# Kernel tuning notes

Measured on AMD Instinct MI355X. Metric: run time of the kernel, lower is better.

## Reference

```python
import jax, jax.numpy as jnp
import numpy as np

B, T, D, H, K = 128, 128, 2048, 512, 512
KSIZES = (2, 3, 4, 5)
OUT_DIM = 2048
IN_DIM = 2 * H + len(KSIZES) * K + D  # 5120
BN_EPS = 1e-5


def _gru_dir(x, w_ih, w_hh, b_ih, b_hh):
    """Single-direction torch-style GRU. x: [B,T,D] -> [B,T,H]."""
    xw = jnp.einsum('btd,gd->btg', x, w_ih) + b_ih  # precompute input proj [B,T,3H]
    h0 = jnp.zeros((x.shape[0], w_hh.shape[1]), x.dtype)

    def step(h, xw_t):
        gh = h @ w_hh.T + b_hh
        xr, xz, xn = jnp.split(xw_t, 3, axis=-1)
        hr, hz, hn = jnp.split(gh, 3, axis=-1)
        r = jax.nn.sigmoid(xr + hr)
        z = jax.nn.sigmoid(xz + hz)
        n = jnp.tanh(xn + r * hn)
        h_new = (1.0 - z) * n + z * h
        return h_new, h_new

    _, hs = jax.lax.scan(step, h0, jnp.swapaxes(xw, 0, 1))
    return jnp.swapaxes(hs, 0, 1)


def _forward(videos, videos_origin, videos_mask, lengths,
             w_ih_f, w_hh_f, b_ih_f, b_hh_f,
             w_ih_b, w_hh_b, b_ih_b, b_hh_b,
             conv_w2, conv_b2, conv_w3, conv_b3, conv_w4, conv_b4, conv_w5, conv_b5,
             fc_w, fc_b, bn_gamma, bn_beta, bn_mean, bn_var):
    # bidirectional GRU on the full padded sequence (torch code does NOT pack)
    fwd = _gru_dir(videos, w_ih_f, w_hh_f, b_ih_f, b_hh_f)
    bwd = _gru_dir(videos[:, ::-1], w_ih_b, w_hh_b, b_ih_b, b_hh_b)[:, ::-1]
    gru_init = jnp.concatenate([fwd, bwd], axis=-1)  # [B,T,2H]

    # fused masked mean (replaces per-sample python loop): mean over first lengths[i] steps
    masked = gru_init * videos_mask[:, :, None]
    mean_gru = masked.sum(axis=1) / lengths.astype(gru_init.dtype)[:, None]  # [B,2H]

    # multi-scale text-CNN over masked GRU outputs
    x4 = masked[:, None, :, :]  # [B,1,T,2H]
    cons = []
    for w, cw, cb in zip(KSIZES, (conv_w2, conv_w3, conv_w4, conv_w5),
                         (conv_b2, conv_b3, conv_b4, conv_b5)):
        y = jax.lax.conv_general_dilated(
            x4, cw, window_strides=(1, 1), padding=[(w - 1, w - 1), (0, 0)],
            dimension_numbers=('NCHW', 'OIHW', 'NCHW'))  # [B,K,T+w-1,1]
        y = jax.nn.relu(y + cb[None, :, None, None])
        cons.append(y.max(axis=(2, 3)))  # global max-pool over time
    con_out = jnp.concatenate(cons, axis=1)  # [B, 4K]

    # concate == 'full' ; dropout is identity at inference
    feats = jnp.concatenate([mean_gru, con_out, videos_origin], axis=1)  # [B,5120]
    feats = feats @ fc_w + fc_b
    feats = bn_gamma * (feats - bn_mean) / jnp.sqrt(bn_var + BN_EPS) + bn_beta
    # l2norm over feature dim
    feats = feats / jnp.sqrt(jnp.sum(feats * feats, axis=1, keepdims=True))
    return feats


def setup_inputs() -> dict:
    key = jax.random.key(0)
    ks = jax.random.split(key, 32)
    s = 0.02
    inp = {
        'videos': jax.random.normal(ks[0], (B, T, D), jnp.float32),
        'videos_origin': jax.random.normal(ks[1], (B, D), jnp.float32),
    }
    lengths = jax.random.randint(ks[2], (B,), 1, T + 1).astype(jnp.int64)
    inp['lengths'] = lengths
    inp['videos_mask'] = (jnp.arange(T)[None, :] < lengths[:, None]).astype(jnp.float32)
    inp['w_ih_f'] = jax.random.normal(ks[3], (3 * H, D), jnp.float32) * s
    inp['w_hh_f'] = jax.random.normal(ks[4], (3 * H, H), jnp.float32) * s
    inp['b_ih_f'] = jnp.zeros((3 * H,), jnp.float32)
    inp['b_hh_f'] = jnp.zeros((3 * H,), jnp.float32)
    inp['w_ih_b'] = jax.random.normal(ks[5], (3 * H, D), jnp.float32) * s
    inp['w_hh_b'] = jax.random.normal(ks[6], (3 * H, H), jnp.float32) * s
    inp['b_ih_b'] = jnp.zeros((3 * H,), jnp.float32)
    inp['b_hh_b'] = jnp.zeros((3 * H,), jnp.float32)
    for i, w in enumerate(KSIZES):
        inp[f'conv_w{w}'] = jax.random.normal(ks[7 + i], (K, 1, w, 2 * H), jnp.float32) * s
        inp[f'conv_b{w}'] = jnp.zeros((K,), jnp.float32)
    inp['fc_w'] = jax.random.normal(ks[12], (IN_DIM, OUT_DIM), jnp.float32) * s
    inp['fc_b'] = jnp.zeros((OUT_DIM,), jnp.float32)
    inp['bn_gamma'] = jnp.ones((OUT_DIM,), jnp.float32)
    inp['bn_beta'] = jnp.zeros((OUT_DIM,), jnp.float32)
    inp['bn_mean'] = jnp.zeros((OUT_DIM,), jnp.float32)
    inp['bn_var'] = jnp.ones((OUT_DIM,), jnp.float32)
    return inp


def reference(videos, videos_origin, lengths, videos_mask,
              w_ih_f, w_hh_f, b_ih_f, b_hh_f,
              w_ih_b, w_hh_b, b_ih_b, b_hh_b,
              conv_w2, conv_b2, conv_w3, conv_b3, conv_w4, conv_b4, conv_w5, conv_b5,
              fc_w, fc_b, bn_gamma, bn_beta, bn_mean, bn_var):
    return _forward(videos, videos_origin, videos_mask, lengths,
                    w_ih_f, w_hh_f, b_ih_f, b_hh_f,
                    w_ih_b, w_hh_b, b_ih_b, b_hh_b,
                    conv_w2, conv_b2, conv_w3, conv_b3, conv_w4, conv_b4, conv_w5, conv_b5,
                    fc_w, fc_b, bn_gamma, bn_beta, bn_mean, bn_var)
```

## Files before the change

### kernel.cpp

```cpp
#include <hip/hip_runtime.h>
#include <stdint.h>

#define B_   128
#define T_   128
#define D_   2048
#define H_   512
#define G3   1536
#define CH   1024
#define KC   512
#define OUTD 2048
#define IND  5120
#define TP   168
#define MPAD 160

typedef short vb8 __attribute__((ext_vector_type(8)));
typedef float v4f __attribute__((ext_vector_type(4)));

__device__ __forceinline__ unsigned short f2b(float f) {
  unsigned u = __float_as_uint(f);
  u = (u + 0x7FFFu + ((u >> 16) & 1u)) >> 16;
  return (unsigned short)u;
}
__device__ __forceinline__ float b2f(unsigned short u) {
  return __uint_as_float((unsigned)u << 16);
}

__device__ __forceinline__ void gl16(const unsigned short* g, unsigned short* l) {
  __builtin_amdgcn_global_load_lds(
      (const __attribute__((address_space(1))) void*)g,
      (__attribute__((address_space(3))) void*)l, 16, 0, 0);
}

__global__ void k_cvt(const float* __restrict__ in, unsigned short* __restrict__ out, int n4) {
  int stride = gridDim.x * blockDim.x;
  for (int i = blockIdx.x * blockDim.x + threadIdx.x; i < n4; i += stride) {
    float4 v = reinterpret_cast<const float4*>(in)[i];
    ushort4 o;
    o.x = f2b(v.x); o.y = f2b(v.y); o.z = f2b(v.z); o.w = f2b(v.w);
    reinterpret_cast<ushort4*>(out)[i] = o;
  }
}

__global__ void k_tcvt(const float* __restrict__ in, unsigned short* __restrict__ out) {
  __shared__ float tile[32][33];
  const int tx = threadIdx.x & 31;
  const int ty = threadIdx.x >> 5;
  const int n0 = blockIdx.x * 32;
  const int k0 = blockIdx.y * 32;
#pragma unroll
  for (int i = 0; i < 4; ++i)
    tile[ty + 8 * i][tx] = in[(size_t)(k0 + ty + 8 * i) * OUTD + n0 + tx];
  __syncthreads();
#pragma unroll
  for (int i = 0; i < 4; ++i)
    out[(size_t)(n0 + ty + 8 * i) * IND + k0 + tx] = f2b(tile[tx][ty + 8 * i]);
}

template<int EPI, int CB>
__global__ __launch_bounds__(256) void k_gemm(
    const unsigned short* __restrict__ A,
    const unsigned short* __restrict__ Bm,
    const float* __restrict__ bias,
    void* __restrict__ Cv,
    int K, int lda, int ldc, int convw)
{
  __shared__ unsigned short sA[128 * 32];
  __shared__ unsigned short sB[128 * 32];
  float*          C32 = (float*)Cv;
  unsigned short* C16 = (unsigned short*)Cv;

  const int m0 = blockIdx.x * 128;
  const int n0 = blockIdx.y * 128;

  const int tid  = threadIdx.x;
  const int lane = tid & 63;
  const int wv   = tid >> 6;
  const int wr   = wv >> 1;
  const int wc   = wv & 1;

  const unsigned short* ag[2];
  const unsigned short* bg[2];
  unsigned short* al[2];
  unsigned short* bl[2];
#pragma unroll
  for (int q = 0; q < 2; ++q) {
    int c  = wv * 2 + q;
    int r  = c * 16 + (lane >> 2);
    int kc = (lane & 3) * 8;
    long abase;
    if (EPI == 1) {
      int m   = m0 + r;
      int b   = m / MPAD;
      int tau = m - b * MPAD;
      abase = (long)(b * TP + 4 + tau - (convw - 1)) * CH;
    } else {
      abase = (long)(m0 + r) * lda;
    }
    ag[q] = A + abase + kc;
    bg[q] = Bm + (long)(n0 + r) * K + kc;
    al[q] = sA + c * 512;
    bl[q] = sB + c * 512;
  }

  v4f acc[4][4] = {};
  const int kq = (lane >> 4) * 8;
  const int fr = lane & 15;

  for (int k0 = 0; k0 < K; k0 += 32) {
    if (k0) __syncthreads();
#pragma unroll
    for (int q = 0; q < 2; ++q) {
      gl16(ag[q] + k0, al[q]);
      gl16(bg[q] + k0, bl[q]);
    }
    __syncthreads();
    vb8 af[4], bfr[4];
#pragma unroll
    for (int i = 0; i < 4; ++i) {
      af[i]  = *reinterpret_cast<const vb8*>(sA + (wr * 64 + i * 16 + fr) * 32 + kq);
      bfr[i] = *reinterpret_cast<const vb8*>(sB + (wc * 64 + i * 16 + fr) * 32 + kq);
    }
#pragma unroll
    for (int i = 0; i < 4; ++i)
#pragma unroll
      for (int j = 0; j < 4; ++j)
        acc[i][j] = __builtin_amdgcn_mfma_f32_16x16x32_bf16(af[i], bfr[j], acc[i][j], 0, 0, 0);
  }

  const int rl = lane >> 4;
#pragma unroll
  for (int i = 0; i < 4; ++i) {
#pragma unroll
    for (int j = 0; j < 4; ++j) {
      int col = n0 + wc * 64 + j * 16 + fr;
      float bs = bias[col];
      if (EPI == 0) {
#pragma unroll
        for (int r = 0; r < 4; ++r) {
          int m = m0 + wr * 64 + i * 16 + rl * 4 + r;
          float v = acc[i][j][r] + bs;
          if (CB) C16[(long)m * ldc + col] = f2b(v);
          else    C32[(long)m * ldc + col] = v;
        }
      } else if (EPI == 2) {
        const int dirb = col >= G3;
        const int xcol = col - dirb * G3;
        unsigned short* base = C16 + (size_t)dirb * ((size_t)B_ * T_ * G3);
#pragma unroll
        for (int r = 0; r < 4; ++r) {
          int m = m0 + wr * 64 + i * 16 + rl * 4 + r;
          base[(long)m * G3 + xcol] = f2b(acc[i][j][r] + bs);
        }
      } else {
        int mf = m0 + wr * 64 + i * 16;
        int b  = mf / MPAD;
        int tf = mf - b * MPAD;
        float mx = 0.f;
#pragma unroll
        for (int r = 0; r < 4; ++r) {
          int tau = tf + rl * 4 + r;
          float v = acc[i][j][r] + bs;
          v = v > 0.f ? v : 0.f;
          if (tau < T_ + convw - 1) mx = v > mx ? v : mx;
        }
        mx = fmaxf(mx, __shfl_xor(mx, 16));
        mx = fmaxf(mx, __shfl_xor(mx, 32));
        if (rl == 0 && tf < T_ + convw - 1)
          atomicMax(reinterpret_cast<int*>(C32 + (long)b * ldc + col), __float_as_int(mx));
      }
    }
  }
}

__global__ __launch_bounds__(512) void k_scan(
    const unsigned short* __restrict__ whh16,
    const float* __restrict__ bhhf, const float* __restrict__ bhhb,
    const unsigned short* __restrict__ xw,
    const int* __restrict__ lengths,
    unsigned short* __restrict__ hbuf,
    unsigned short* __restrict__ xpad,
    float* __restrict__ meang,
    unsigned int* __restrict__ cnt)
{
  __shared__ unsigned short sw[96 * 512];
  const int wg   = blockIdx.x;
  const int dir  = wg >> 4;
  const int u0   = (wg & 15) * 32;
  const int tid  = threadIdx.x;
  const int lane = tid & 63;
  const int wv   = tid >> 6;
  const int fr   = lane & 15;
  const int rl   = lane >> 4;
  const int kq   = rl * 8;

  const unsigned short* Wd  = whh16 + (size_t)dir * (3 * H_ * H_);
  const float*          bhh = dir ? bhhb : bhhf;
  const unsigned short* xwd = xw + (size_t)dir * ((size_t)B_ * T_ * G3);
  unsigned short* hb = hbuf + dir * (2 * B_ * H_);
  unsigned int* mycnt = cnt + dir * 64;

  for (int i = tid; i < 96 * 64; i += 512) {
    int row  = i >> 6;
    int slot = i & 63;
    const unsigned short* src = Wd + (size_t)((row >> 5) * H_ + u0 + (row & 31)) * H_ + slot * 8;
    *reinterpret_cast<vb8*>((char*)sw + ((row * 1024 + slot * 16) ^ ((row & 7) << 4))) =
        *reinterpret_cast<const vb8*>(src);
  }
  __syncthreads();

  int mylen[4];
#pragma unroll
  for (int r = 0; r < 4; ++r) mylen[r] = lengths[wv * 16 + rl * 4 + r];

  float bh[3][2];
#pragma unroll
  for (int g = 0; g < 3; ++g)
#pragma unroll
    for (int j = 0; j < 2; ++j) bh[g][j] = bhh[g * H_ + u0 + j * 16 + fr];

  float hst[8], macc[8];
#pragma unroll
  for (int i = 0; i < 8; ++i) { hst[i] = 0.f; macc[i] = 0.f; }

  unsigned short uxw[3][2][4];
  {
    const int t0 = dir ? (T_ - 1) : 0;
#pragma unroll
    for (int g = 0; g < 3; ++g)
#pragma unroll
      for (int j = 0; j < 2; ++j)
#pragma unroll
        for (int r = 0; r < 4; ++r)
          uxw[g][j][r] = xwd[((size_t)(wv * 16 + rl * 4 + r) * T_ + t0) * G3 +
                             g * H_ + u0 + j * 16 + fr];
  }

  for (int s = 0; s < T_; ++s) {
    const int t = dir ? (T_ - 1 - s) : s;

    v4f acc[3][2] = {};
    if (s > 0) {
      const unsigned short* arow = hb + ((s - 1) & 1) * (B_ * H_) + (wv * 16 + fr) * H_;
#pragma unroll 4
      for (int ks = 0; ks < 16; ++ks) {
        vb8 a = *reinterpret_cast<const vb8*>(arow + ks * 32 + kq);
#pragma unroll
        for (int g = 0; g < 3; ++g)
#pragma unroll
          for (int j = 0; j < 2; ++j) {
            vb8 wf = *reinterpret_cast<const vb8*>(
                (const char*)sw +
                (((g * 32 + j * 16 + fr) * 1024 + ks * 64 + rl * 16) ^ ((fr & 7) << 4)));
            acc[g][j] = __builtin_amdgcn_mfma_f32_16x16x32_bf16(a, wf, acc[g][j], 0, 0, 0);
          }
      }
    }

    unsigned short* hc = hb + (s & 1) * (B_ * H_);
#pragma unroll
    for (int j = 0; j < 2; ++j)
#pragma unroll
      for (int r = 0; r < 4; ++r) {
        const int idx = j * 4 + r;
        const int b   = wv * 16 + rl * 4 + r;
        const int u   = u0 + j * 16 + fr;
        float xr = b2f(uxw[0][j][r]), xz = b2f(uxw[1][j][r]), xn = b2f(uxw[2][j][r]);
        float hr = acc[0][j][r] + bh[0][j];
        float hz = acc[1][j][r] + bh[1][j];
        float hn = acc[2][j][r] + bh[2][j];
        float rr = 1.f / (1.f + __expf(-(xr + hr)));
        float z  = 1.f / (1.f + __expf(-(xz + hz)));
        float ax = xn + rr * hn;
        float n  = 2.f / (1.f + __expf(-2.f * ax)) - 1.f;
        float h  = (1.f - z) * n + z * hst[idx];
        hst[idx] = h;
        hc[b * H_ + u] = f2b(h);
        if (t < mylen[r]) {
          xpad[((size_t)b * TP + 4 + t) * CH + dir * H_ + u] = f2b(h);
          macc[idx] += h;
        }
      }

    if (s < T_ - 1) {
      const int tn = dir ? (T_ - 2 - s) : (s + 1);
#pragma unroll
      for (int g = 0; g < 3; ++g)
#pragma unroll
        for (int j = 0; j < 2; ++j)
#pragma unroll
          for (int r = 0; r < 4; ++r)
            uxw[g][j][r] = xwd[((size_t)(wv * 16 + rl * 4 + r) * T_ + tn) * G3 +
                               g * H_ + u0 + j * 16 + fr];
      __syncthreads();
      if (tid == 0) {
        __hip_atomic_fetch_add(mycnt, 1u, __ATOMIC_RELEASE, __HIP_MEMORY_SCOPE_AGENT);
        const unsigned tgt = (unsigned)(s + 1) * 16;
        while (__hip_atomic_load(mycnt, __ATOMIC_RELAXED, __HIP_MEMORY_SCOPE_AGENT) < tgt)
          __builtin_amdgcn_s_sleep(1);
        __builtin_amdgcn_fence(__ATOMIC_ACQUIRE, "agent");
      }
      __syncthreads();
    }
  }

#pragma unroll
  for (int j = 0; j < 2; ++j)
#pragma unroll
    for (int r = 0; r < 4; ++r)
      meang[(size_t)(wv * 16 + rl * 4 + r) * CH + dir * H_ + u0 + j * 16 + fr] =
          macc[j * 4 + r] / (float)mylen[r];
}

__global__ void k_feats(const float* __restrict__ mg, const float* __restrict__ co,
                        const float* __restrict__ vo, unsigned short* __restrict__ out) {
  int i = blockIdx.x * 256 + threadIdx.x;
  int b = i / IND, c = i - b * IND;
  float v;
  if (c < CH) v = mg[b * CH + c];
  else if (c < CH + OUTD) v = co[b * OUTD + (c - CH)];
  else v = vo[b * D_ + (c - CH - OUTD)];
  out[i] = f2b(v);
}

__global__ __launch_bounds__(256) void k_bnnorm(const float* __restrict__ x,
    const float* __restrict__ g, const float* __restrict__ bt,
    const float* __restrict__ mn, const float* __restrict__ vr,
    float* __restrict__ out) {
  const int b = blockIdx.x;
  __shared__ float red[4];
  float vals[8];
  float ss = 0.f;
#pragma unroll
  for (int i = 0; i < 8; ++i) {
    int c = threadIdx.x + i * 256;
    float y = g[c] * (x[(size_t)b * OUTD + c] - mn[c]) / sqrtf(vr[c] + 1e-5f) + bt[c];
    vals[i] = y;
    ss += y * y;
  }
#pragma unroll
  for (int s2 = 1; s2 < 64; s2 <<= 1) ss += __shfl_xor(ss, s2);
  if ((threadIdx.x & 63) == 0) red[threadIdx.x >> 6] = ss;
  __syncthreads();
  float inv = 1.f / sqrtf(red[0] + red[1] + red[2] + red[3]);
#pragma unroll
  for (int i = 0; i < 8; ++i)
    out[(size_t)b * OUTD + threadIdx.x + i * 256] = vals[i] * inv;
}

extern "C" void kernel_launch(void* const* d_in, const int* in_sizes, int n_in,
                              void* d_out, int out_size, void* d_ws, size_t ws_size,
                              hipStream_t stream) {
  (void)in_sizes; (void)n_in; (void)out_size; (void)ws_size;
  const float* videos = (const float*)d_in[0];
  const float* vorig  = (const float*)d_in[1];
  const int*   lens   = (const int*)d_in[2];
  const float* wihf = (const float*)d_in[4];
  const float* whhf = (const float*)d_in[5];
  const float* bihf = (const float*)d_in[6];
  const float* bhhf = (const float*)d_in[7];
  const float* wihb = (const float*)d_in[8];
  const float* whhb = (const float*)d_in[9];
  const float* bihb = (const float*)d_in[10];
  const float* bhhb = (const float*)d_in[11];
  const float* cw[4] = {(const float*)d_in[12], (const float*)d_in[14],
                        (const float*)d_in[16], (const float*)d_in[18]};
  const float* cb[4] = {(const float*)d_in[13], (const float*)d_in[15],
                        (const float*)d_in[17], (const float*)d_in[19]};
  const float* fcw = (const float*)d_in[20];
  const float* fcb = (const float*)d_in[21];
  const float* bng = (const float*)d_in[22];
  const float* bnb = (const float*)d_in[23];
  const float* bnm = (const float*)d_in[24];
  const float* bnv = (const float*)d_in[25];
  float* out = (float*)d_out;

  char* ws = (char*)d_ws;
  size_t off = 0;
  auto alloc = [&](size_t bytes) -> void* {
    void* p = ws + off;
    off = (off + bytes + 255) & ~(size_t)255;
    return p;
  };
  unsigned int*   cnt    = (unsigned int*)alloc(1024);
  unsigned short* xw16   = (unsigned short*)alloc((size_t)2 * B_ * T_ * G3 * 2);
  unsigned short* whh16  = (unsigned short*)alloc((size_t)2 * 3 * H_ * H_ * 2);
  unsigned short* hbuf   = (unsigned short*)alloc((size_t)2 * 2 * B_ * H_ * 2);
  float*          meang  = (float*)alloc((size_t)B_ * CH * 4);
  float*          conout = (float*)alloc((size_t)B_ * OUTD * 4);
  unsigned short* feats  = (unsigned short*)alloc((size_t)B_ * IND * 2);
  float*          fcout  = (float*)alloc((size_t)B_ * OUTD * 4);
  unsigned short* wihcat = (unsigned short*)alloc((size_t)2 * G3 * D_ * 2);
  unsigned short* cw16   = (unsigned short*)alloc((size_t)KC * 14 * CH * 2);
  unsigned short* vid16  = (unsigned short*)alloc((size_t)B_ * T_ * D_ * 2);
  float*          biascat= (float*)alloc(2 * G3 * 4);
  unsigned short* xpad = vid16;
  unsigned short* fcT  = vid16 + (size_t)B_ * TP * CH;

  hipMemsetAsync(cnt, 0, 1024, stream);
  hipMemsetAsync(conout, 0, (size_t)B_ * OUTD * 4, stream);
  hipMemcpyAsync(biascat,      bihf, G3 * 4, hipMemcpyDeviceToDevice, stream);
  hipMemcpyAsync(biascat + G3, bihb, G3 * 4, hipMemcpyDeviceToDevice, stream);

  k_cvt<<<2048, 256, 0, stream>>>(videos, vid16, B_ * T_ * D_ / 4);
  k_cvt<<<512, 256, 0, stream>>>(wihf, wihcat, G3 * D_ / 4);
  k_cvt<<<512, 256, 0, stream>>>(wihb, wihcat + (size_t)G3 * D_, G3 * D_ / 4);
  k_cvt<<<768, 256, 0, stream>>>(whhf, whh16, 3 * H_ * H_ / 4);
  k_cvt<<<768, 256, 0, stream>>>(whhb, whh16 + (size_t)3 * H_ * H_, 3 * H_ * H_ / 4);
  {
    size_t cwoff = 0;
    for (int i = 0; i < 4; ++i) {
      int w = i + 2;
      int n = KC * w * CH;
      k_cvt<<<256, 256, 0, stream>>>(cw[i], cw16 + cwoff, n / 4);
      cwoff += (size_t)n;
    }
  }

  k_gemm<2, 1><<<dim3(128, 24), 256, 0, stream>>>(vid16, wihcat, biascat, xw16, D_, D_, 0, 0);

  hipMemsetAsync(xpad, 0, (size_t)B_ * TP * CH * 2, stream);
  k_tcvt<<<dim3(64, 160), 256, 0, stream>>>(fcw, fcT);

  k_scan<<<dim3(32), dim3(512), 0, stream>>>(whh16, bhhf, bhhb, xw16, lens,
                                             hbuf, xpad, meang, cnt);

  {
    size_t cwoff = 0;
    for (int i = 0; i < 4; ++i) {
      int w = i + 2;
      k_gemm<1, 0><<<dim3(160, 4), 256, 0, stream>>>(xpad, cw16 + cwoff, cb[i],
                                                     conout + i * KC, w * CH, 0, OUTD, w);
      cwoff += (size_t)KC * w * CH;
    }
  }

  k_feats<<<2560, 256, 0, stream>>>(meang, conout, vorig, feats);
  k_gemm<0, 0><<<dim3(1, 16), 256, 0, stream>>>(feats, fcT, fcb, fcout, IND, IND, OUTD, 0);
  k_bnnorm<<<B_, 256, 0, stream>>>(fcout, bng, bnb, bnm, bnv, out);
}
```

Before: 1.934 ms.

## Batch conv GEMMs into one launch, trim padding, split-K the FC GEMM

The four text-CNN conv GEMM launches become a single launch, with grid z selecting the kernel width, its weight offset and a concatenated bias. The per-sample row padding drops from 160 to 144, which still covers T+w-1 for every width and cuts wasted tile rows. The FC GEMM, which ran on only 16 workgroups, now splits K four ways into separate fp32 partial buffers. The batchnorm/normalize kernel sums those partials and adds the FC bias, at the cost of extra partial-buffer traffic.

Result: faster. 1.830 ms (-5.4%).

```diff
diff --git a/kernel.cpp b/kernel.cpp
--- a/kernel.cpp
+++ b/kernel.cpp
@@ -11,7 +11,7 @@
 #define OUTD 2048
 #define IND  5120
 #define TP   168
-#define MPAD 160
+#define MPAD 144
 
 typedef short vb8 __attribute__((ext_vector_type(8)));
 typedef float v4f __attribute__((ext_vector_type(4)));
@@ -71,6 +71,23 @@
 
   const int m0 = blockIdx.x * 128;
   const int n0 = blockIdx.y * 128;
+  const int cz = blockIdx.z;
+
+  int K_ = K;
+  int w_ = convw;
+  int koff = 0;
+  const unsigned short* Bm_ = Bm;
+  const float* bias_ = bias;
+  if (EPI == 1) {
+    constexpr int cum[4] = {0, 2, 5, 9};
+    w_   = cz + 2;
+    K_   = w_ * CH;
+    Bm_  = Bm + (size_t)cum[cz] * KC * CH;
+    bias_ = bias + cz * KC;
+  } else if (EPI == 3) {
+    koff = cz * K;
+  }
+  const int bstride = (EPI == 3) ? convw : K_;
 
   const int tid  = threadIdx.x;
   const int lane = tid & 63;
@@ -92,12 +109,12 @@
       int m   = m0 + r;
       int b   = m / MPAD;
       int tau = m - b * MPAD;
-      abase = (long)(b * TP + 4 + tau - (convw - 1)) * CH;
+      abase = (long)(b * TP + 4 + tau - (w_ - 1)) * CH;
     } else {
-      abase = (long)(m0 + r) * lda;
+      abase = (long)(m0 + r) * lda + koff;
     }
     ag[q] = A + abase + kc;
-    bg[q] = Bm + (long)(n0 + r) * K + kc;
+    bg[q] = Bm_ + (long)(n0 + r) * bstride + kc + koff;
     al[q] = sA + c * 512;
     bl[q] = sB + c * 512;
   }
@@ -106,7 +123,7 @@
   const int kq = (lane >> 4) * 8;
   const int fr = lane & 15;
 
-  for (int k0 = 0; k0 < K; k0 += 32) {
+  for (int k0 = 0; k0 < K_; k0 += 32) {
     if (k0) __syncthreads();
 #pragma unroll
     for (int q = 0; q < 2; ++q) {
@@ -133,7 +150,7 @@
 #pragma unroll
     for (int j = 0; j < 4; ++j) {
       int col = n0 + wc * 64 + j * 16 + fr;
-      float bs = bias[col];
+      float bs = (EPI == 3) ? 0.f : bias_[col];
       if (EPI == 0) {
 #pragma unroll
         for (int r = 0; r < 4; ++r) {
@@ -151,6 +168,12 @@
           int m = m0 + wr * 64 + i * 16 + rl * 4 + r;
           base[(long)m * G3 + xcol] = f2b(acc[i][j][r] + bs);
         }
+      } else if (EPI == 3) {
+#pragma unroll
+        for (int r = 0; r < 4; ++r) {
+          int m = m0 + wr * 64 + i * 16 + rl * 4 + r;
+          C32[(size_t)cz * (B_ * OUTD) + (long)m * ldc + col] = acc[i][j][r];
+        }
       } else {
         int mf = m0 + wr * 64 + i * 16;
         int b  = mf / MPAD;
@@ -161,12 +184,13 @@
           int tau = tf + rl * 4 + r;
           float v = acc[i][j][r] + bs;
           v = v > 0.f ? v : 0.f;
-          if (tau < T_ + convw - 1) mx = v > mx ? v : mx;
+          if (tau < T_ + w_ - 1) mx = v > mx ? v : mx;
         }
         mx = fmaxf(mx, __shfl_xor(mx, 16));
         mx = fmaxf(mx, __shfl_xor(mx, 32));
-        if (rl == 0 && tf < T_ + convw - 1)
-          atomicMax(reinterpret_cast<int*>(C32 + (long)b * ldc + col), __float_as_int(mx));
+        if (rl == 0 && tf < T_ + w_ - 1)
+          atomicMax(reinterpret_cast<int*>(C32 + (long)b * ldc + cz * KC + col),
+                    __float_as_int(mx));
       }
     }
   }
@@ -323,17 +347,21 @@
 }
 
 __global__ __launch_bounds__(256) void k_bnnorm(const float* __restrict__ x,
+    const float* __restrict__ fcb,
     const float* __restrict__ g, const float* __restrict__ bt,
     const float* __restrict__ mn, const float* __restrict__ vr,
     float* __restrict__ out) {
   const int b = blockIdx.x;
+  const size_t PL = (size_t)B_ * OUTD;
   __shared__ float red[4];
   float vals[8];
   float ss = 0.f;
 #pragma unroll
   for (int i = 0; i < 8; ++i) {
     int c = threadIdx.x + i * 256;
-    float y = g[c] * (x[(size_t)b * OUTD + c] - mn[c]) / sqrtf(vr[c] + 1e-5f) + bt[c];
+    size_t o = (size_t)b * OUTD + c;
+    float xs = x[o] + x[PL + o] + x[2 * PL + o] + x[3 * PL + o] + fcb[c];
+    float y = g[c] * (xs - mn[c]) / sqrtf(vr[c] + 1e-5f) + bt[c];
     vals[i] = y;
     ss += y * y;
   }
@@ -388,11 +416,12 @@
   float*          meang  = (float*)alloc((size_t)B_ * CH * 4);
   float*          conout = (float*)alloc((size_t)B_ * OUTD * 4);
   unsigned short* feats  = (unsigned short*)alloc((size_t)B_ * IND * 2);
-  float*          fcout  = (float*)alloc((size_t)B_ * OUTD * 4);
+  float*          fcpart = (float*)alloc((size_t)4 * B_ * OUTD * 4);
   unsigned short* wihcat = (unsigned short*)alloc((size_t)2 * G3 * D_ * 2);
   unsigned short* cw16   = (unsigned short*)alloc((size_t)KC * 14 * CH * 2);
   unsigned short* vid16  = (unsigned short*)alloc((size_t)B_ * T_ * D_ * 2);
   float*          biascat= (float*)alloc(2 * G3 * 4);
+  float*          cbcat  = (float*)alloc(4 * KC * 4);
   unsigned short* xpad = vid16;
   unsigned short* fcT  = vid16 + (size_t)B_ * TP * CH;
 
@@ -400,6 +429,8 @@
   hipMemsetAsync(conout, 0, (size_t)B_ * OUTD * 4, stream);
   hipMemcpyAsync(biascat,      bihf, G3 * 4, hipMemcpyDeviceToDevice, stream);
   hipMemcpyAsync(biascat + G3, bihb, G3 * 4, hipMemcpyDeviceToDevice, stream);
+  for (int i = 0; i < 4; ++i)
+    hipMemcpyAsync(cbcat + i * KC, cb[i], KC * 4, hipMemcpyDeviceToDevice, stream);
 
   k_cvt<<<2048, 256, 0, stream>>>(videos, vid16, B_ * T_ * D_ / 4);
   k_cvt<<<512, 256, 0, stream>>>(wihf, wihcat, G3 * D_ / 4);
@@ -424,17 +455,10 @@
   k_scan<<<dim3(32), dim3(512), 0, stream>>>(whh16, bhhf, bhhb, xw16, lens,
                                              hbuf, xpad, meang, cnt);
 
-  {
-    size_t cwoff = 0;
-    for (int i = 0; i < 4; ++i) {
-      int w = i + 2;
-      k_gemm<1, 0><<<dim3(160, 4), 256, 0, stream>>>(xpad, cw16 + cwoff, cb[i],
-                                                     conout + i * KC, w * CH, 0, OUTD, w);
-      cwoff += (size_t)KC * w * CH;
-    }
-  }
+  k_gemm<1, 0><<<dim3(144, 4, 4), 256, 0, stream>>>(xpad, cw16, cbcat, conout, 0, 0, OUTD, 0);
 
   k_feats<<<2560, 256, 0, stream>>>(meang, conout, vorig, feats);
-  k_gemm<0, 0><<<dim3(1, 16), 256, 0, stream>>>(feats, fcT, fcb, fcout, IND, IND, OUTD, 0);
-  k_bnnorm<<<B_, 256, 0, stream>>>(fcout, bng, bnb, bnm, bnv, out);
-}
+  k_gemm<3, 0><<<dim3(1, 16, 4), 256, 0, stream>>>(feats, fcT, fcb, fcpart,
+                                                   IND / 4, IND, OUTD, IND);
+  k_bnnorm<<<B_, 256, 0, stream>>>(fcpart, fcb, bng, bnb, bnm, bnv, out);
+}
```
